# Optimization experiments

Measured on AMD Instinct MI355X. Metric: run time of the kernel, lower is better.

The kernel has to match this reference:

```python
import jax, jax.numpy as jnp
import numpy as np

B, K, C = 2, 128, 256
IMG = 512
OH = OW = 16


def setup_inputs():
    key = jax.random.key(0)
    ks = jax.random.split(key, 10)

    def _coords(k1, k2):
        lo = jax.random.uniform(k1, (B, K), minval=0.0, maxval=IMG * 0.6)
        ln = jax.random.uniform(k2, (B, K), minval=8.0, maxval=IMG * 0.35)
        return lo, jnp.minimum(lo + ln, float(IMG))

    y1, y2 = _coords(ks[0], ks[1])
    x1, x2 = _coords(ks[2], ks[3])
    bboxess = jnp.stack([y1, x1, y2, x2], axis=-1)  # [B,K,4] valid boxes
    counts = jax.random.randint(ks[4], (B, 1), K // 2, K + 1).astype(jnp.int32)
    mk = lambda k, h: jax.random.normal(k, (B, C, h, h), jnp.float32)
    return {"bboxess": bboxess, "counts": counts,
            "p2": mk(ks[5], 128), "p3": mk(ks[6], 64), "p4": mk(ks[7], 32),
            "p5": mk(ks[8], 16), "p6": mk(ks[9], 8),
            "img_h": IMG, "img_w": IMG}


def _roi_align(bboxess, counts, p2, p3, p4, p5, p6, img_h, img_w):
    # Faithful fused form of: upsample level map to (img_h,img_w) bilinear
    # (align_corners=False), crop rounded box, bilinear-resize crop to 16x16.
    # Bilinear is separable, so each output pixel touches <=4 level rows/cols;
    # we gather those taps directly instead of materializing the full-res map.
    Bn, Kn, _ = bboxess.shape
    H2, W2 = p2.shape[2], p2.shape[3]
    pad = lambda p: jnp.pad(p, ((0, 0), (0, 0), (0, H2 - p.shape[2]), (0, W2 - p.shape[3])))
    # calc_level clamps to [2,5] => p6 never selected
    P = jnp.stack([p2, pad(p3), pad(p4), pad(p5)], axis=1)  # [B,4,C,H2,W2]
    sizes_h = jnp.array([p2.shape[2], p3.shape[2], p4.shape[2], p5.shape[2]], jnp.int32)
    sizes_w = jnp.array([p2.shape[3], p3.shape[3], p4.shape[3], p5.shape[3]], jnp.int32)
    img_area = float(img_h * img_w)

    def taps(n_out, start, crop_len, p_size, img_size):
        # stage 2: output bin -> pair of full-res integer pixels (torch rule:
        # src = max(0, scale*(dst+0.5)-0.5), neighbor clamped to edge)
        o = jnp.arange(n_out, dtype=jnp.float32)
        s = jnp.maximum((o + 0.5) * crop_len.astype(jnp.float32) / n_out - 0.5, 0.0)
        f0 = jnp.floor(s)
        w1 = s - f0
        f0i = f0.astype(jnp.int32)
        f1i = jnp.minimum(f0i + 1, crop_len - 1)

        def to_level(f):
            # stage 1: full-res pixel -> pair of level-map pixels
            g = jnp.maximum((f.astype(jnp.float32) + 0.5) * p_size.astype(jnp.float32) / img_size - 0.5, 0.0)
            g0 = jnp.floor(g)
            v = g - g0
            g0i = g0.astype(jnp.int32)
            g1i = jnp.minimum(g0i + 1, p_size - 1)
            return g0i, g1i, v

        a0, a1, va = to_level(start + f0i)
        b0, b1, vb = to_level(start + f1i)
        idx = jnp.stack([a0, a1, b0, b1], axis=1)  # [n_out,4] level indices
        wt = jnp.stack([(1.0 - w1) * (1.0 - va), (1.0 - w1) * va,
                        w1 * (1.0 - vb), w1 * vb], axis=1)  # [n_out,4]
        return idx, wt

    def box_fn(Pb, bbox):  # Pb: [4,C,H2,W2], bbox: [4]
        y1f, x1f, y2f, x2f = bbox[0], bbox[1], bbox[2], bbox[3]
        area = (y2f - y1f) * (x2f - x1f)
        lvl = jnp.clip(jnp.round(6.0 + jnp.log2(jnp.sqrt(area) / jnp.sqrt(img_area))), 2, 5).astype(jnp.int32) - 2
        ph, pw = sizes_h[lvl], sizes_w[lvl]
        bi = jnp.round(bbox).astype(jnp.int32)
        y1 = jnp.clip(bi[0], 0, img_h - 1)
        x1 = jnp.clip(bi[1], 0, img_w - 1)
        y2 = jnp.clip(bi[2], y1 + 1, img_h)
        x2 = jnp.clip(bi[3], x1 + 1, img_w)
        Iy, Wy = taps(OH, y1, y2 - y1, ph, float(img_h))
        Ix, Wx = taps(OW, x1, x2 - x1, pw, float(img_w))
        Pl = Pb[lvl]  # [C,H2,W2] (levels zero-padded to p2 size)
        out = jnp.zeros((Pl.shape[0], OH, OW), Pl.dtype)
        for a in range(4):  # fixed 4x4 separable taps
            for b in range(4):
                w = Wy[:, a][:, None] * Wx[:, b][None, :]  # [OH,OW]
                out = out + w * Pl[:, Iy[:, a][:, None], Ix[:, b][None, :]]
        return out  # [C,OH,OW]

    per_batch = jax.vmap(box_fn, in_axes=(None, 0))
    out = jax.vmap(per_batch, in_axes=(0, 0))(P, bboxess)  # [B,K,C,OH,OW]
    valid = (jnp.arange(Kn)[None, :] < counts).astype(out.dtype)  # [B,K]
    return out * valid[:, :, None, None, None]


def reference(bboxess, counts, p2, p3, p4, p5, p6, img_h, img_w):
    return _roi_align(bboxess, counts, p2, p3, p4, p5, p6, img_h, img_w)
```

## Files before the change

kernel.cpp:

```cpp
#include <hip/hip_runtime.h>
#include <math.h>


constexpr int Bn = 2, Kn = 128, Cn = 256;
constexpr int CSPLIT = 8;
constexpr int CCH = Cn / CSPLIT;
constexpr int MAXPX = 240;

__device__ __forceinline__ float levelg(int F, int psize) {
  return fmaxf(((float)F + 0.5f) * (float)psize * (1.0f / 512.0f) - 0.5f, 0.0f);
}

__device__ __forceinline__ void to_level(int F, int psize,
                                         int& g0i, int& g1i, float& v) {
  float g = levelg(F, psize);
  float g0 = floorf(g);
  v = g - g0;
  g0i = (int)g0;
  g1i = min(g0i + 1, psize - 1);
}

__device__ __forceinline__ void to_level_pair(int F, int psize,
                                              int& base, float& wlo, float& whi) {
  float g = levelg(F, psize);
  float g0 = floorf(g);
  float v = g - g0;
  int g0i = (int)g0;
  if (g0i >= psize - 1) { base = psize - 2; wlo = 0.0f; whi = 1.0f; }
  else                  { base = g0i;       wlo = 1.0f - v; whi = v; }
}

__device__ __forceinline__ int pair_base(int F, int psize) {
  return min((int)floorf(levelg(F, psize)), psize - 2);
}

__device__ __forceinline__ void bin_f(int o, int crop,
                                      int& f0i, int& f1i, float& w1) {
  float s = fmaxf(((float)o + 0.5f) * (float)crop * (1.0f / 16.0f) - 0.5f, 0.0f);
  float f0 = floorf(s);
  w1 = s - f0;
  f0i = (int)f0;
  f1i = min(f0i + 1, crop - 1);
}

__device__ __forceinline__ float2 load_f2(const float* p) {
  float2 v;
  __builtin_memcpy(&v, p, 8);
  return v;
}

__global__ __launch_bounds__(256, 5)
void roialign_kernel(const float* __restrict__ bbox,
                     const int* __restrict__ counts,
                     const float* __restrict__ p2,
                     const float* __restrict__ p3,
                     const float* __restrict__ p4,
                     const float* __restrict__ p5,
                     float* __restrict__ out) {
  __shared__ float smem[CCH * MAXPX];

  const int blk = blockIdx.x;
  const int cpart = blk & (CSPLIT - 1);
  const int box = blk / CSPLIT;
  const int b = box >> 7;
  const int k = box & 127;
  const int t = threadIdx.x;
  const int oy = t >> 4, ox = t & 15;

  const long outBase = ((long)box * Cn + cpart * CCH) * 256 + t;

  if (k >= counts[b]) {
    for (int c = 0; c < CCH; ++c) out[outBase + (long)c * 256] = 0.0f;
    return;
  }

  const float y1f = bbox[box * 4 + 0], x1f = bbox[box * 4 + 1];
  const float y2f = bbox[box * 4 + 2], x2f = bbox[box * 4 + 3];
  const float area = (y2f - y1f) * (x2f - x1f);
  const int lvl = (area > 2048.0f) + (area >= 8192.0f) + (area > 32768.0f);
  const int ph = 128 >> lvl;
  const int pw = ph;

  const int y1 = min(max((int)rintf(y1f), 0), 511);
  const int x1 = min(max((int)rintf(x1f), 0), 511);
  const int y2 = min(max((int)rintf(y2f), y1 + 1), 512);
  const int x2 = min(max((int)rintf(x2f), x1 + 1), 512);
  const int cropy = y2 - y1, cropx = x2 - x1;

  int iyr[4];
  float wyr[4];
  {
    int f0i, f1i; float w1;
    bin_f(oy, cropy, f0i, f1i, w1);
    int a0, a1, b0, b1; float va, vb;
    to_level(y1 + f0i, ph, a0, a1, va);
    to_level(y1 + f1i, ph, b0, b1, vb);
    iyr[0] = a0; iyr[1] = a1; iyr[2] = b0; iyr[3] = b1;
    wyr[0] = (1.0f - w1) * (1.0f - va);
    wyr[1] = (1.0f - w1) * va;
    wyr[2] = w1 * (1.0f - vb);
    wyr[3] = w1 * vb;
  }

  int bx[2];
  float wxl[2], wxh[2];
  {
    int f0i, f1i; float w1;
    bin_f(ox, cropx, f0i, f1i, w1);
    float l0, h0, l1, h1;
    to_level_pair(x1 + f0i, pw, bx[0], l0, h0);
    to_level_pair(x1 + f1i, pw, bx[1], l1, h1);
    wxl[0] = (1.0f - w1) * l0; wxh[0] = (1.0f - w1) * h0;
    wxl[1] = w1 * l1;          wxh[1] = w1 * h1;
  }

  int y_lo, y_hi, x_lo, x_hi;
  {
    int f0a, f1a, f0b, f1b; float wd;
    bin_f(0, cropy, f0a, f1a, wd);
    bin_f(15, cropy, f0b, f1b, wd);
    int g0, g1; float vd;
    to_level(y1 + f0a, ph, g0, g1, vd); y_lo = g0;
    to_level(y1 + f1b, ph, g0, g1, vd); y_hi = g1;
    bin_f(0, cropx, f0a, f1a, wd);
    bin_f(15, cropx, f0b, f1b, wd);
    x_lo = pair_base(x1 + f0a, pw);
    x_hi = pair_base(x1 + f1b, pw) + 1;
  }
  const int ey = y_hi - y_lo + 1;
  const int ex = x_hi - x_lo + 1;
  const int ex_pad = ex | 1;
  const int region = ey * ex;

  const float* Pbase;
  switch (lvl) {
    case 0: Pbase = p2; break;
    case 1: Pbase = p3; break;
    case 2: Pbase = p4; break;
    default: Pbase = p5; break;
  }
  const int planeStride = ph * pw;
  const float* plane = Pbase + ((long)b * Cn + cpart * CCH) * planeStride;

  if (ey * ex_pad > MAXPX) {
    int off[8];
    float wl[8], wh[8];
#pragma unroll
    for (int r = 0; r < 4; ++r)
#pragma unroll
      for (int p = 0; p < 2; ++p) {
        off[r * 2 + p] = iyr[r] * pw + bx[p];
        wl[r * 2 + p] = wyr[r] * wxl[p];
        wh[r * 2 + p] = wyr[r] * wxh[p];
      }
    for (int c = 0; c < CCH; ++c) {
      const float* __restrict__ P = plane + (long)c * planeStride;
      float acc = 0.0f;
#pragma unroll
      for (int i = 0; i < 8; ++i) {
        const float2 v = load_f2(P + off[i]);
        acc = fmaf(wl[i], v.x, acc);
        acc = fmaf(wh[i], v.y, acc);
      }
      out[outBase + (long)c * 256] = acc;
    }
    return;
  }

  {
    const bool act = (t < region);
    int sr = 0, sx = 0;
    if (act) { sr = t / ex; sx = t - sr * ex; }
    const int gsrc = (y_lo + sr) * pw + (x_lo + sx);
    const int ldst = sr * ex_pad + sx;
    if (act) {
#pragma unroll 4
      for (int c = 0; c < CCH; ++c)
        smem[c * MAXPX + ldst] = plane[(long)c * planeStride + gsrc];
    }
  }
  __syncthreads();

  int loff[8];
  float wl[8], wh[8];
#pragma unroll
  for (int r = 0; r < 4; ++r)
#pragma unroll
    for (int p = 0; p < 2; ++p) {
      loff[r * 2 + p] = (iyr[r] - y_lo) * ex_pad + (bx[p] - x_lo);
      wl[r * 2 + p] = wyr[r] * wxl[p];
      wh[r * 2 + p] = wyr[r] * wxh[p];
    }

  for (int c = 0; c < CCH; ++c) {
    const float* __restrict__ base = smem + c * MAXPX;
    float acc = 0.0f;
#pragma unroll
    for (int i = 0; i < 8; ++i) {
      acc = fmaf(wl[i], base[loff[i]], acc);
      acc = fmaf(wh[i], base[loff[i] + 1], acc);
    }
    out[outBase + (long)c * 256] = acc;
  }
}

extern "C" void kernel_launch(void* const* d_in, const int* in_sizes, int n_in,
                              void* d_out, int out_size, void* d_ws, size_t ws_size,
                              hipStream_t stream) {
  const float* bbox = (const float*)d_in[0];
  const int* counts = (const int*)d_in[1];
  const float* p2 = (const float*)d_in[2];
  const float* p3 = (const float*)d_in[3];
  const float* p4 = (const float*)d_in[4];
  const float* p5 = (const float*)d_in[5];
  float* out = (float*)d_out;

  dim3 grid(Bn * Kn * CSPLIT);
  dim3 block(256);
  roialign_kernel<<<grid, block, 0, stream>>>(bbox, counts, p2, p3, p4, p5, out);
}
```

Measured before the change: 123.8 us.

## Split channels 16 ways, flatten smem staging loop, interleave two channels

Doubles the channel split so each block handles 16 channels, giving 4096 blocks and half the shared memory per block, and raises the occupancy hint to 8 blocks per CU. The shared-memory fill now walks a flattened (channel, pixel) index with all 256 threads instead of only threads below the region size, so staging work is spread evenly across the block. The compute loop handles two channels per iteration with independent accumulators to expose more ILP. Costs are integer divisions in the staging loop, more per-block setup overhead, and a tighter register budget.

Measured after the change: 124.2 us. No clear change (+0.3%).

```diff
diff --git a/kernel.cpp b/kernel.cpp
--- a/kernel.cpp
+++ b/kernel.cpp
@@ -3,7 +3,7 @@
 
 
 constexpr int Bn = 2, Kn = 128, Cn = 256;
-constexpr int CSPLIT = 8;
+constexpr int CSPLIT = 16;
 constexpr int CCH = Cn / CSPLIT;
 constexpr int MAXPX = 240;
 
@@ -49,7 +49,7 @@
   return v;
 }
 
-__global__ __launch_bounds__(256, 5)
+__global__ __launch_bounds__(256, 8)
 void roialign_kernel(const float* __restrict__ bbox,
                      const int* __restrict__ counts,
                      const float* __restrict__ p2,
@@ -70,6 +70,7 @@
   const long outBase = ((long)box * Cn + cpart * CCH) * 256 + t;
 
   if (k >= counts[b]) {
+#pragma unroll 4
     for (int c = 0; c < CCH; ++c) out[outBase + (long)c * 256] = 0.0f;
     return;
   }
@@ -168,15 +169,14 @@
   }
 
   {
-    const bool act = (t < region);
-    int sr = 0, sx = 0;
-    if (act) { sr = t / ex; sx = t - sr * ex; }
-    const int gsrc = (y_lo + sr) * pw + (x_lo + sx);
-    const int ldst = sr * ex_pad + sx;
-    if (act) {
-#pragma unroll 4
-      for (int c = 0; c < CCH; ++c)
-        smem[c * MAXPX + ldst] = plane[(long)c * planeStride + gsrc];
+    const int total = region * CCH;
+    for (int e = t; e < total; e += 256) {
+      const int c = e / region;
+      const int px = e - c * region;
+      const int sr = px / ex;
+      const int sx = px - sr * ex;
+      smem[c * MAXPX + sr * ex_pad + sx] =
+          plane[(long)c * planeStride + (y_lo + sr) * pw + (x_lo + sx)];
     }
   }
   __syncthreads();
@@ -192,15 +192,19 @@
       wh[r * 2 + p] = wyr[r] * wxh[p];
     }
 
-  for (int c = 0; c < CCH; ++c) {
-    const float* __restrict__ base = smem + c * MAXPX;
-    float acc = 0.0f;
+  for (int c = 0; c < CCH; c += 2) {
+    const float* __restrict__ b0 = smem + c * MAXPX;
+    const float* __restrict__ b1 = b0 + MAXPX;
+    float a0 = 0.0f, a1 = 0.0f;
 #pragma unroll
     for (int i = 0; i < 8; ++i) {
-      acc = fmaf(wl[i], base[loff[i]], acc);
-      acc = fmaf(wh[i], base[loff[i] + 1], acc);
-    }
-    out[outBase + (long)c * 256] = acc;
+      a0 = fmaf(wl[i], b0[loff[i]], a0);
+      a0 = fmaf(wh[i], b0[loff[i] + 1], a0);
+      a1 = fmaf(wl[i], b1[loff[i]], a1);
+      a1 = fmaf(wh[i], b1[loff[i] + 1], a1);
+    }
+    out[outBase + (long)c * 256] = a0;
+    out[outBase + (long)(c + 1) * 256] = a1;
   }
 }
 
```

## Apply separable bilinear as x-pass into shared rows then y-pass

Applied to the files above, without the earlier changes.

Replaces the staged 2D patch with a separable two-pass scheme. Each thread first computes the x-interpolated value for its output column across all needed level rows and stores it in shared memory. It then combines four row values with the y weights. The channel split grows from 8 to 32 so each block handles fewer channels and the grid gets more blocks. The aim is to cut shared-memory reads and per-channel FMAs and to allow tall boxes to stay on the shared path. The cost is redundant global loads across blocks and a smaller per-block workload.

Measured after the change: 135.2 us. +9.2%, slower.

```diff
diff --git a/kernel.cpp b/kernel.cpp
--- a/kernel.cpp
+++ b/kernel.cpp
@@ -3,9 +3,11 @@
 
 
 constexpr int Bn = 2, Kn = 128, Cn = 256;
-constexpr int CSPLIT = 8;
+constexpr int CSPLIT = 32;
 constexpr int CCH = Cn / CSPLIT;
-constexpr int MAXPX = 240;
+constexpr int MAXROWS = 50;
+constexpr int XSTR = 17;
+constexpr int XCH = MAXROWS * XSTR;
 
 __device__ __forceinline__ float levelg(int F, int psize) {
   return fmaxf(((float)F + 0.5f) * (float)psize * (1.0f / 512.0f) - 0.5f, 0.0f);
@@ -30,10 +32,6 @@
   else                  { base = g0i;       wlo = 1.0f - v; whi = v; }
 }
 
-__device__ __forceinline__ int pair_base(int F, int psize) {
-  return min((int)floorf(levelg(F, psize)), psize - 2);
-}
-
 __device__ __forceinline__ void bin_f(int o, int crop,
                                       int& f0i, int& f1i, float& w1) {
   float s = fmaxf(((float)o + 0.5f) * (float)crop * (1.0f / 16.0f) - 0.5f, 0.0f);
@@ -57,11 +55,11 @@
                      const float* __restrict__ p4,
                      const float* __restrict__ p5,
                      float* __restrict__ out) {
-  __shared__ float smem[CCH * MAXPX];
+  __shared__ float X[CCH * XCH];
 
   const int blk = blockIdx.x;
   const int cpart = blk & (CSPLIT - 1);
-  const int box = blk / CSPLIT;
+  const int box = blk >> 5;
   const int b = box >> 7;
   const int k = box & 127;
   const int t = threadIdx.x;
@@ -70,6 +68,7 @@
   const long outBase = ((long)box * Cn + cpart * CCH) * 256 + t;
 
   if (k >= counts[b]) {
+#pragma unroll
     for (int c = 0; c < CCH; ++c) out[outBase + (long)c * 256] = 0.0f;
     return;
   }
@@ -87,34 +86,34 @@
   const int x2 = min(max((int)rintf(x2f), x1 + 1), 512);
   const int cropy = y2 - y1, cropx = x2 - x1;
 
-  int iyr[4];
+  int a0, b0;
   float wyr[4];
   {
     int f0i, f1i; float w1;
     bin_f(oy, cropy, f0i, f1i, w1);
-    int a0, a1, b0, b1; float va, vb;
-    to_level(y1 + f0i, ph, a0, a1, va);
-    to_level(y1 + f1i, ph, b0, b1, vb);
-    iyr[0] = a0; iyr[1] = a1; iyr[2] = b0; iyr[3] = b1;
+    int ga0, ga1, gb0, gb1; float va, vb;
+    to_level(y1 + f0i, ph, ga0, ga1, va);
+    to_level(y1 + f1i, ph, gb0, gb1, vb);
+    a0 = ga0; b0 = gb0;
     wyr[0] = (1.0f - w1) * (1.0f - va);
     wyr[1] = (1.0f - w1) * va;
     wyr[2] = w1 * (1.0f - vb);
     wyr[3] = w1 * vb;
   }
 
-  int bx[2];
-  float wxl[2], wxh[2];
+  int bx0, bx1;
+  float wxl0, wxh0, wxl1, wxh1;
   {
     int f0i, f1i; float w1;
     bin_f(ox, cropx, f0i, f1i, w1);
     float l0, h0, l1, h1;
-    to_level_pair(x1 + f0i, pw, bx[0], l0, h0);
-    to_level_pair(x1 + f1i, pw, bx[1], l1, h1);
-    wxl[0] = (1.0f - w1) * l0; wxh[0] = (1.0f - w1) * h0;
-    wxl[1] = w1 * l1;          wxh[1] = w1 * h1;
-  }
-
-  int y_lo, y_hi, x_lo, x_hi;
+    to_level_pair(x1 + f0i, pw, bx0, l0, h0);
+    to_level_pair(x1 + f1i, pw, bx1, l1, h1);
+    wxl0 = (1.0f - w1) * l0; wxh0 = (1.0f - w1) * h0;
+    wxl1 = w1 * l1;          wxh1 = w1 * h1;
+  }
+
+  int y_lo, y_hi;
   {
     int f0a, f1a, f0b, f1b; float wd;
     bin_f(0, cropy, f0a, f1a, wd);
@@ -122,15 +121,8 @@
     int g0, g1; float vd;
     to_level(y1 + f0a, ph, g0, g1, vd); y_lo = g0;
     to_level(y1 + f1b, ph, g0, g1, vd); y_hi = g1;
-    bin_f(0, cropx, f0a, f1a, wd);
-    bin_f(15, cropx, f0b, f1b, wd);
-    x_lo = pair_base(x1 + f0a, pw);
-    x_hi = pair_base(x1 + f1b, pw) + 1;
-  }
-  const int ey = y_hi - y_lo + 1;
-  const int ex = x_hi - x_lo + 1;
-  const int ex_pad = ex | 1;
-  const int region = ey * ex;
+  }
+  const int nrows = y_hi - y_lo + 2;
 
   const float* Pbase;
   switch (lvl) {
@@ -142,64 +134,58 @@
   const int planeStride = ph * pw;
   const float* plane = Pbase + ((long)b * Cn + cpart * CCH) * planeStride;
 
-  if (ey * ex_pad > MAXPX) {
-    int off[8];
-    float wl[8], wh[8];
-#pragma unroll
-    for (int r = 0; r < 4; ++r)
-#pragma unroll
-      for (int p = 0; p < 2; ++p) {
-        off[r * 2 + p] = iyr[r] * pw + bx[p];
-        wl[r * 2 + p] = wyr[r] * wxl[p];
-        wh[r * 2 + p] = wyr[r] * wxh[p];
-      }
+  if (nrows > MAXROWS) {
     for (int c = 0; c < CCH; ++c) {
       const float* __restrict__ P = plane + (long)c * planeStride;
       float acc = 0.0f;
-#pragma unroll
-      for (int i = 0; i < 8; ++i) {
-        const float2 v = load_f2(P + off[i]);
-        acc = fmaf(wl[i], v.x, acc);
-        acc = fmaf(wh[i], v.y, acc);
-      }
+      const float2 va0 = load_f2(P + a0 * pw + bx0);
+      const float2 va1 = load_f2(P + a0 * pw + bx1);
+      const float2 vA0 = load_f2(P + min(a0 + 1, ph - 1) * pw + bx0);
+      const float2 vA1 = load_f2(P + min(a0 + 1, ph - 1) * pw + bx1);
+      const float2 vb0 = load_f2(P + b0 * pw + bx0);
+      const float2 vb1 = load_f2(P + b0 * pw + bx1);
+      const float2 vB0 = load_f2(P + min(b0 + 1, ph - 1) * pw + bx0);
+      const float2 vB1 = load_f2(P + min(b0 + 1, ph - 1) * pw + bx1);
+      acc = fmaf(wyr[0] * wxl0, va0.x, acc); acc = fmaf(wyr[0] * wxh0, va0.y, acc);
+      acc = fmaf(wyr[0] * wxl1, va1.x, acc); acc = fmaf(wyr[0] * wxh1, va1.y, acc);
+      acc = fmaf(wyr[1] * wxl0, vA0.x, acc); acc = fmaf(wyr[1] * wxh0, vA0.y, acc);
+      acc = fmaf(wyr[1] * wxl1, vA1.x, acc); acc = fmaf(wyr[1] * wxh1, vA1.y, acc);
+      acc = fmaf(wyr[2] * wxl0, vb0.x, acc); acc = fmaf(wyr[2] * wxh0, vb0.y, acc);
+      acc = fmaf(wyr[2] * wxl1, vb1.x, acc); acc = fmaf(wyr[2] * wxh1, vb1.y, acc);
+      acc = fmaf(wyr[3] * wxl0, vB0.x, acc); acc = fmaf(wyr[3] * wxh0, vB0.y, acc);
+      acc = fmaf(wyr[3] * wxl1, vB1.x, acc); acc = fmaf(wyr[3] * wxh1, vB1.y, acc);
       out[outBase + (long)c * 256] = acc;
     }
     return;
   }
 
   {
-    const bool act = (t < region);
-    int sr = 0, sx = 0;
-    if (act) { sr = t / ex; sx = t - sr * ex; }
-    const int gsrc = (y_lo + sr) * pw + (x_lo + sx);
-    const int ldst = sr * ex_pad + sx;
-    if (act) {
-#pragma unroll 4
-      for (int c = 0; c < CCH; ++c)
-        smem[c * MAXPX + ldst] = plane[(long)c * planeStride + gsrc];
+    const int rlane = t >> 4;
+#pragma unroll 2
+    for (int c = 0; c < CCH; ++c) {
+      const float* __restrict__ P = plane + (long)c * planeStride;
+      float* __restrict__ Xc = X + c * XCH;
+      for (int r = rlane; r < nrows; r += 16) {
+        const int srow = min(y_lo + r, ph - 1);
+        const float* __restrict__ row = P + srow * pw;
+        const float2 v0 = load_f2(row + bx0);
+        const float2 v1 = load_f2(row + bx1);
+        Xc[r * XSTR + ox] =
+            fmaf(wxh1, v1.y, fmaf(wxl1, v1.x, fmaf(wxh0, v0.y, wxl0 * v0.x)));
+      }
     }
   }
   __syncthreads();
 
-  int loff[8];
-  float wl[8], wh[8];
-#pragma unroll
-  for (int r = 0; r < 4; ++r)
-#pragma unroll
-    for (int p = 0; p < 2; ++p) {
-      loff[r * 2 + p] = (iyr[r] - y_lo) * ex_pad + (bx[p] - x_lo);
-      wl[r * 2 + p] = wyr[r] * wxl[p];
-      wh[r * 2 + p] = wyr[r] * wxh[p];
-    }
-
+  const int oa = (a0 - y_lo) * XSTR + ox;
+  const int ob = (b0 - y_lo) * XSTR + ox;
+#pragma unroll 2
   for (int c = 0; c < CCH; ++c) {
-    const float* __restrict__ base = smem + c * MAXPX;
-    float acc = 0.0f;
-#pragma unroll
-    for (int i = 0; i < 8; ++i) {
-      acc = fmaf(wl[i], base[loff[i]], acc);
-      acc = fmaf(wh[i], base[loff[i] + 1], acc);
-    }
+    const float* __restrict__ Xc = X + c * XCH;
+    float acc = wyr[0] * Xc[oa];
+    acc = fmaf(wyr[1], Xc[oa + XSTR], acc);
+    acc = fmaf(wyr[2], Xc[ob], acc);
+    acc = fmaf(wyr[3], Xc[ob + XSTR], acc);
     out[outBase + (long)c * 256] = acc;
   }
 }
```
